# Optimization experiments

Measured on AMD Instinct MI355X. Metric: run time of the kernel, lower is better.

## Reference

```python
import jax, jax.numpy as jnp
import numpy as np
import math

B, C, H, W = 32, 128, 32, 32
NUM_HEADS = 4
GROUPS = 32
EPS = 1e-5


def setup_inputs() -> dict:
    key = jax.random.key(0)
    ks = jax.random.split(key, 6)
    x = jax.random.normal(ks[0], (B, C, H, W), jnp.float32)
    norm_w = 1.0 + 0.1 * jax.random.normal(ks[1], (C,), jnp.float32)
    norm_b = 0.1 * jax.random.normal(ks[2], (C,), jnp.float32)
    qkv_w = jax.random.normal(ks[3], (3 * C, C), jnp.float32) / math.sqrt(C)
    proj_w = jax.random.normal(ks[4], (C, C), jnp.float32) / math.sqrt(C)
    proj_b = 0.01 * jax.random.normal(ks[5], (C,), jnp.float32)
    return {"x": x, "norm_w": norm_w, "norm_b": norm_b, "qkv_w": qkv_w,
            "proj_w": proj_w, "proj_b": proj_b}


def _group_norm(x, w, b):
    b_, c, h, w_ = x.shape
    xg = x.reshape(b_, GROUPS, c // GROUPS, h, w_)
    mu = xg.mean(axis=(2, 3, 4), keepdims=True)
    var = xg.var(axis=(2, 3, 4), keepdims=True)
    xn = ((xg - mu) * jax.lax.rsqrt(var + EPS)).reshape(b_, c, h, w_)
    return xn * w[None, :, None, None] + b[None, :, None, None]


def reference(x, norm_w, norm_b, qkv_w, proj_w, proj_b):
    b, c, h, w = x.shape
    nh = NUM_HEADS
    dh = c // nh
    hw = h * w
    xn = _group_norm(x, norm_w, norm_b)
    # 1x1 conv (no bias): [B,3C,H,W] flattened to [B,3C,HW]
    qkv = jnp.einsum('oc,bchw->bohw', qkv_w, xn).reshape(b, nh, 3 * dh, hw)
    # torch reshape (B*nh, 3C/nh, HW) + chunk(3, dim=1): per-head interleave
    q, k, v = qkv[:, :, :dh], qkv[:, :, dh:2 * dh], qkv[:, :, 2 * dh:]
    scale = 1.0 / math.sqrt(dh)
    # scale applied to BOTH q and k, as in the source
    attn = jnp.einsum('bhct,bhcs->bhts', q * scale, k * scale)  # [B,nh,HW,HW]
    attn = jax.nn.softmax(attn, axis=-1)
    hout = jnp.einsum('bhts,bhcs->bhct', attn, v).reshape(b, c, h, w)
    hout = jnp.einsum('oc,bchw->bohw', proj_w, hout) + proj_b[None, :, None, None]
    return hout + x
```

## Files before the change

kernel.cpp:

```cpp
#include <hip/hip_runtime.h>
#include <math.h>

#define BB 32
#define CC 128
#define HW 1024
#define NG 32
#define TPG 4096
#define QSZ ((size_t)BB * 4 * HW * 32)

typedef __attribute__((ext_vector_type(8))) short fragAB;
typedef __attribute__((ext_vector_type(4))) float fragC;
typedef __attribute__((ext_vector_type(8))) ushort ushort8v;

__device__ __forceinline__ ushort f2bf(float f) {
  union { float f; uint u; } v; v.f = f;
  uint r = v.u + 0x7FFFu + ((v.u >> 16) & 1u);
  return (ushort)(r >> 16);
}
__device__ __forceinline__ uint pack2(float lo, float hi) {
  return __builtin_amdgcn_perm(__float_as_uint(hi), __float_as_uint(lo), 0x07060302u);
}
__device__ __forceinline__ float bflo(uint u) { return __uint_as_float(u << 16); }
__device__ __forceinline__ float bfhi(uint u) { return __uint_as_float(u & 0xffff0000u); }
__device__ __forceinline__ int vswz(int row, int g) {
  return row * 128 + 16 * (g ^ (row & 7));
}

__global__ __launch_bounds__(256) void gn_stats(const float* __restrict__ x,
    float2* __restrict__ stats, const float* __restrict__ qkvw,
    const float* __restrict__ projw, ushort* __restrict__ wq16,
    ushort* __restrict__ wp16) {
  if (blockIdx.x >= 1024) {
    int idx = (blockIdx.x - 1024) * 256 + threadIdx.x;
    if (idx < 49152) wq16[idx] = f2bf(qkvw[idx]);
    else             wp16[idx - 49152] = f2bf(projw[idx - 49152]);
    return;
  }
  int blk = blockIdx.x;
  int b = blk >> 5, g = blk & 31;
  const float4* xp4 = (const float4*)(x + ((size_t)(b * CC + g * 4)) * HW);
  float s = 0.f, s2 = 0.f;
  #pragma unroll
  for (int i = 0; i < 4; ++i) {
    float4 v = xp4[threadIdx.x + i * 256];
    s  += v.x + v.y + v.z + v.w;
    s2 += v.x * v.x + v.y * v.y + v.z * v.z + v.w * v.w;
  }
  #pragma unroll
  for (int off = 32; off; off >>= 1) {
    s  += __shfl_down(s, off, 64);
    s2 += __shfl_down(s2, off, 64);
  }
  __shared__ float ls[4], ls2[4];
  int lane = threadIdx.x & 63, wid = threadIdx.x >> 6;
  if (lane == 0) { ls[wid] = s; ls2[wid] = s2; }
  __syncthreads();
  if (threadIdx.x == 0) {
    float a  = ls[0] + ls[1] + ls[2] + ls[3];
    float a2 = ls2[0] + ls2[1] + ls2[2] + ls2[3];
    float mu = a * (1.f / TPG);
    float var = a2 * (1.f / TPG) - mu * mu;
    stats[blk] = make_float2(mu, rsqrtf(var + 1e-5f));
  }
}

__global__ __launch_bounds__(256) void mgemm_qkv(
    const ushort* __restrict__ W16, const float* __restrict__ xf,
    const float2* __restrict__ stats, const float* __restrict__ gw,
    const float* __restrict__ gb, ushort* __restrict__ Qb) {
  __shared__ ushort Xs[64 * 128];
  int b = blockIdx.z, t0 = blockIdx.x * 64;
  int tid = threadIdx.x;
  int lane = tid & 63, w = tid >> 6, lc = lane & 15, lg = lane >> 4;
  int wo = w >> 1, wt = w & 1;

  {
    int tq = tid & 15, co = tid >> 4;
    const float* xb = xf + (size_t)b * CC * HW + t0 + tq * 4;
    float wsc[8], bsc[8];
    {
      float2 s0 = stats[b * 32 + co * 2];
      float2 s1 = stats[b * 32 + co * 2 + 1];
      #pragma unroll
      for (int cc = 0; cc < 8; ++cc) {
        float rst = (cc < 4) ? s0.y : s1.y;
        float mu  = (cc < 4) ? s0.x : s1.x;
        float g = gw[co * 8 + cc];
        wsc[cc] = g * rst;
        bsc[cc] = gb[co * 8 + cc] - mu * wsc[cc];
      }
    }
    union { float4 v; float f[4]; } vv[8];
    #pragma unroll
    for (int cc = 0; cc < 8; ++cc)
      vv[cc].v = *(const float4*)&xb[(size_t)(co * 8 + cc) * HW];
    #pragma unroll
    for (int tt = 0; tt < 4; ++tt) {
      int row = tq * 4 + tt;
      ushort8v r;
      #pragma unroll
      for (int cc = 0; cc < 8; ++cc)
        r[cc] = f2bf(vv[cc].f[tt] * wsc[cc] + bsc[cc]);
      int byt = (row * 256 + co * 16) ^ ((row & 7) << 4);
      *(ushort8v*)((char*)Xs + byt) = r;
    }
  }
  __syncthreads();

  auto load_af = [&](fragAB af[2][4], int o0) {
    #pragma unroll
    for (int i = 0; i < 2; ++i)
      #pragma unroll
      for (int kc = 0; kc < 4; ++kc)
        af[i][kc] = *(const fragAB*)&W16[(size_t)(o0 + wo * 32 + i * 16 + lc) * 128 + kc * 32 + lg * 8];
  };
  auto kloop = [&](fragAB af[2][4], fragC acc[2][2]) {
    #pragma unroll
    for (int i = 0; i < 2; ++i)
      #pragma unroll
      for (int j = 0; j < 2; ++j)
        acc[i][j] = (fragC){0.f, 0.f, 0.f, 0.f};
    #pragma unroll
    for (int kc = 0; kc < 4; ++kc) {
      fragAB bf[2];
      #pragma unroll
      for (int j = 0; j < 2; ++j) {
        int row = wt * 32 + j * 16 + lc;
        int byt = (row * 256 + kc * 64 + lg * 16) ^ ((row & 7) << 4);
        bf[j] = *(const fragAB*)((const char*)Xs + byt);
      }
      #pragma unroll
      for (int i = 0; i < 2; ++i)
        #pragma unroll
        for (int j = 0; j < 2; ++j)
          acc[i][j] = __builtin_amdgcn_mfma_f32_16x16x32_bf16(af[i][kc], bf[j], acc[i][j], 0, 0, 0);
    }
  };
  auto epi = [&](fragC acc[2][2], int o0) {
    #pragma unroll
    for (int i = 0; i < 2; ++i) {
      int ob = o0 + wo * 32 + i * 16;
      int blk = ob >> 5;
      int hh = blk / 3, kind = blk % 3;
      size_t bh = (size_t)b * 4 + hh;
      float sc = (kind == 0) ? (0.03125f * 1.44269504f) : 1.f;
      #pragma unroll
      for (int j = 0; j < 2; ++j) {
        if (kind < 2) {
          ushort* dst = (kind == 0) ? Qb : (Qb + QSZ);
          int s16 = (t0 >> 4) + wt * 2 + j;
          int eo = s16 * 512 + (((ob & 16) >> 3) + (lg >> 1)) * 128 + lc * 8 + (lg & 1) * 4;
          ushort4 rv;
          rv.x = f2bf(acc[i][j][0] * sc); rv.y = f2bf(acc[i][j][1] * sc);
          rv.z = f2bf(acc[i][j][2] * sc); rv.w = f2bf(acc[i][j][3] * sc);
          *(ushort4*)&dst[bh * 32768 + eo] = rv;
        } else {
          ushort* Vb = Qb + 2 * QSZ;
          int eo = (t0 >> 6) * 2048 + ((ob & 16) >> 4) * 1024
                 + (wt * 4 + j * 2 + (lc >> 3)) * 128 + (lc & 7);
          #pragma unroll
          for (int r = 0; r < 4; ++r)
            Vb[bh * 32768 + eo + (lg * 4 + r) * 8] = f2bf(acc[i][j][r]);
        }
      }
    }
  };

  fragAB afA[2][4], afB[2][4];
  fragC acc[2][2];
  load_af(afA, 0);
  load_af(afB, 64);
  kloop(afA, acc); epi(acc, 0);   load_af(afA, 128);
  kloop(afB, acc); epi(acc, 64);  load_af(afB, 192);
  kloop(afA, acc); epi(acc, 128); load_af(afA, 256);
  kloop(afB, acc); epi(acc, 192); load_af(afB, 320);
  kloop(afA, acc); epi(acc, 256);
  kloop(afB, acc); epi(acc, 320);
}

__global__ __launch_bounds__(512) void attn8(
    const ushort* __restrict__ Qb, const ushort* __restrict__ Kb,
    const ushort* __restrict__ Vb, const ushort* __restrict__ wp16,
    const float* __restrict__ bias, const float* __restrict__ resid,
    float* __restrict__ out) {
  __shared__ char arena[27136];

  int tid = threadIdx.x;
  int w = tid >> 6, lane = tid & 63, lc = lane & 15, lg = lane >> 4;
  int lb = blockIdx.x;
  int gp = (lb & 7) * 128 + (lb >> 3);
  int b = gp >> 5, qt = gp & 31;
  int h = w >> 1, sh = w & 1;
  int bh = b * 4 + h;
  int t0 = qt * 32;

  const ushort* Qg = Qb + (size_t)bh * 32768 + (size_t)qt * 1024 + lane * 8;
  const ushort* Kg = Kb + (size_t)bh * 32768 + lane * 8;
  const ushort* Vg = Vb + (size_t)bh * 32768 + lane * 8;

  fragAB q0 = *(const fragAB*)&Qg[0];
  fragAB q1 = *(const fragAB*)&Qg[512];

  fragC a00 = {0.f,0.f,0.f,0.f}, a01 = {0.f,0.f,0.f,0.f};
  fragC a10 = {0.f,0.f,0.f,0.f}, a11 = {0.f,0.f,0.f,0.f};
  float l0 = 0.f, l1 = 0.f;
  char* PsB = arena + w * 2048;

  for (int i = sh * 8; i < sh * 8 + 8; ++i) {
    const ushort* Kt = Kg + i * 2048;
    const ushort* Vt = Vg + i * 2048;
    fragAB kf[4], vf[4];
    #pragma unroll
    for (int j = 0; j < 4; ++j) kf[j] = *(const fragAB*)&Kt[j * 512];
    #pragma unroll
    for (int u = 0; u < 4; ++u) vf[u] = *(const fragAB*)&Vt[u * 512];

    #pragma unroll
    for (int ts = 0; ts < 2; ++ts) {
      fragAB qf = ts ? q1 : q0;
      fragC S[4];
      #pragma unroll
      for (int j = 0; j < 4; ++j) {
        fragC z = {0.f,0.f,0.f,0.f};
        S[j] = __builtin_amdgcn_mfma_f32_16x16x32_bf16(kf[j], qf, z, 0, 0, 0);
      }
      float rs = 0.f;
      #pragma unroll
      for (int j = 0; j < 4; ++j) {
        float p0 = __builtin_amdgcn_exp2f(S[j][0]), p1 = __builtin_amdgcn_exp2f(S[j][1]);
        float p2 = __builtin_amdgcn_exp2f(S[j][2]), p3 = __builtin_amdgcn_exp2f(S[j][3]);
        rs += (p0 + p1) + (p2 + p3);
        uint2 wv2;
        wv2.x = pack2(p0, p1);
        wv2.y = pack2(p2, p3);
        int g = j * 2 + (lg >> 1);
        *(uint2*)(PsB + lc * 128 + 16 * (g ^ (lc & 7)) + (lg & 1) * 8) = wv2;
      }
      if (ts) l1 += rs; else l0 += rs;
      fragC* aA = ts ? &a01 : &a00;
      fragC* aB = ts ? &a11 : &a10;
      fragAB bp0 = *(const fragAB*)(PsB + vswz(lc, lg));
      fragAB bp1 = *(const fragAB*)(PsB + vswz(lc, 4 + lg));
      *aA = __builtin_amdgcn_mfma_f32_16x16x32_bf16(vf[0], bp0, *aA, 0, 0, 0);
      *aA = __builtin_amdgcn_mfma_f32_16x16x32_bf16(vf[1], bp1, *aA, 0, 0, 0);
      *aB = __builtin_amdgcn_mfma_f32_16x16x32_bf16(vf[2], bp0, *aB, 0, 0, 0);
      *aB = __builtin_amdgcn_mfma_f32_16x16x32_bf16(vf[3], bp1, *aB, 0, 0, 0);
    }
  }

  float2* lpart = (float2*)(arena + 16384);
  if (sh == 1) {
    char* slot = PsB + lane * 32;
    uint2 u;
    u.x = pack2(a00[0], a00[1]); u.y = pack2(a00[2], a00[3]);
    *(uint2*)(slot) = u;
    u.x = pack2(a10[0], a10[1]); u.y = pack2(a10[2], a10[3]);
    *(uint2*)(slot + 8) = u;
    u.x = pack2(a01[0], a01[1]); u.y = pack2(a01[2], a01[3]);
    *(uint2*)(slot + 16) = u;
    u.x = pack2(a11[0], a11[1]); u.y = pack2(a11[2], a11[3]);
    *(uint2*)(slot + 24) = u;
    lpart[h * 64 + lane] = make_float2(l0, l1);
  }
  __syncthreads();

  ushort* Olds = (ushort*)(arena + 18432);
  if (sh == 0) {
    const char* slot = arena + (w + 1) * 2048 + lane * 32;
    uint2 u0 = *(const uint2*)(slot);
    uint2 u1 = *(const uint2*)(slot + 8);
    uint2 u2 = *(const uint2*)(slot + 16);
    uint2 u3 = *(const uint2*)(slot + 24);
    float2 lv = lpart[h * 64 + lane];
    a00[0] += bflo(u0.x); a00[1] += bfhi(u0.x); a00[2] += bflo(u0.y); a00[3] += bfhi(u0.y);
    a10[0] += bflo(u1.x); a10[1] += bfhi(u1.x); a10[2] += bflo(u1.y); a10[3] += bfhi(u1.y);
    a01[0] += bflo(u2.x); a01[1] += bfhi(u2.x); a01[2] += bflo(u2.y); a01[3] += bfhi(u2.y);
    a11[0] += bflo(u3.x); a11[1] += bfhi(u3.x); a11[2] += bflo(u3.y); a11[3] += bfhi(u3.y);
    l0 += lv.x; l1 += lv.y;

    l0 += __shfl_xor(l0, 16); l0 += __shfl_xor(l0, 32);
    l1 += __shfl_xor(l1, 16); l1 += __shfl_xor(l1, 32);
    float il0 = 1.f / l0, il1 = 1.f / l1;

    int cb = h * 32;
    uint2 u;
    u.x = pack2(a00[0] * il0, a00[1] * il0); u.y = pack2(a00[2] * il0, a00[3] * il0);
    *(uint2*)&Olds[lc * 136 + cb + lg * 4] = u;
    u.x = pack2(a10[0] * il0, a10[1] * il0); u.y = pack2(a10[2] * il0, a10[3] * il0);
    *(uint2*)&Olds[lc * 136 + cb + 16 + lg * 4] = u;
    u.x = pack2(a01[0] * il1, a01[1] * il1); u.y = pack2(a01[2] * il1, a01[3] * il1);
    *(uint2*)&Olds[(lc + 16) * 136 + cb + lg * 4] = u;
    u.x = pack2(a11[0] * il1, a11[1] * il1); u.y = pack2(a11[2] * il1, a11[3] * il1);
    *(uint2*)&Olds[(lc + 16) * 136 + cb + 16 + lg * 4] = u;
  }
  __syncthreads();

  fragC pacc[2] = {{0.f,0.f,0.f,0.f}, {0.f,0.f,0.f,0.f}};
  #pragma unroll
  for (int kc = 0; kc < 4; ++kc) {
    fragAB af = *(const fragAB*)&wp16[(size_t)(16 * w + lc) * 128 + kc * 32 + lg * 8];
    #pragma unroll
    for (int j = 0; j < 2; ++j) {
      fragAB bf = *(const fragAB*)&Olds[(j * 16 + lc) * 136 + kc * 32 + lg * 8];
      pacc[j] = __builtin_amdgcn_mfma_f32_16x16x32_bf16(af, bf, pacc[j], 0, 0, 0);
    }
  }
  #pragma unroll
  for (int j = 0; j < 2; ++j) {
    int t = t0 + j * 16 + lc;
    #pragma unroll
    for (int r = 0; r < 4; ++r) {
      int o = 16 * w + lg * 4 + r;
      size_t idx = ((size_t)b * CC + o) * HW + t;
      out[idx] = pacc[j][r] + bias[o] + resid[idx];
    }
  }
}

extern "C" void kernel_launch(void* const* d_in, const int* in_sizes, int n_in,
                              void* d_out, int out_size, void* d_ws, size_t ws_size,
                              hipStream_t stream) {
  (void)in_sizes; (void)n_in; (void)out_size; (void)ws_size;
  const float* x     = (const float*)d_in[0];
  const float* gw    = (const float*)d_in[1];
  const float* gb    = (const float*)d_in[2];
  const float* qkvw  = (const float*)d_in[3];
  const float* projw = (const float*)d_in[4];
  const float* projb = (const float*)d_in[5];
  float* out = (float*)d_out;

  char* wsb = (char*)d_ws;
  ushort* Qb   = (ushort*)(wsb + ((size_t)8 << 20));
  ushort* Kb   = Qb + QSZ;
  ushort* Vb   = Qb + 2 * QSZ;
  ushort* wq16 = (ushort*)(wsb + ((size_t)32 << 20));
  ushort* wp16 = (ushort*)(wsb + ((size_t)32 << 20) + (128 << 10));
  float2* stats = (float2*)(wsb + ((size_t)32 << 20) + (256 << 10));

  gn_stats<<<dim3(BB * NG + 256), 256, 0, stream>>>(x, stats, qkvw, projw, wq16, wp16);
  mgemm_qkv<<<dim3(16, 1, BB), 256, 0, stream>>>(wq16, x, stats, gw, gb, Qb);
  attn8<<<dim3(1024), 512, 0, stream>>>(Qb, Kb, Vb, wp16, projb, x, out);
}
```

Measured before the change: 60.16 us.

## Split attention work by query tile instead of key halves, halving block count

Each attention block now handles 64 queries per batch element, and its two waves per head each take a different 32-query tile over all 16 key tiles. Previously the two waves of a head split the keys and merged partial results through shared memory. Removing that split drops the bf16 partial-accumulator exchange, the extra barrier and the merge arithmetic, and lets the output projection cover 64 tokens per block. The cost is half as many blocks (512 instead of 1024), each doing twice the serial key-loop work, which may reduce latency hiding and occupancy.

```diff
diff --git a/kernel.cpp b/kernel.cpp
--- a/kernel.cpp
+++ b/kernel.cpp
@@ -20,8 +20,6 @@
 __device__ __forceinline__ uint pack2(float lo, float hi) {
   return __builtin_amdgcn_perm(__float_as_uint(hi), __float_as_uint(lo), 0x07060302u);
 }
-__device__ __forceinline__ float bflo(uint u) { return __uint_as_float(u << 16); }
-__device__ __forceinline__ float bfhi(uint u) { return __uint_as_float(u & 0xffff0000u); }
 __device__ __forceinline__ int vswz(int row, int g) {
   return row * 128 + 16 * (g ^ (row & 7));
 }
@@ -178,21 +176,22 @@
   kloop(afB, acc); epi(acc, 320);
 }
 
-__global__ __launch_bounds__(512) void attn8(
+__global__ __launch_bounds__(512) void attn9(
     const ushort* __restrict__ Qb, const ushort* __restrict__ Kb,
     const ushort* __restrict__ Vb, const ushort* __restrict__ wp16,
     const float* __restrict__ bias, const float* __restrict__ resid,
     float* __restrict__ out) {
-  __shared__ char arena[27136];
+  __shared__ char arena[33792];
 
   int tid = threadIdx.x;
   int w = tid >> 6, lane = tid & 63, lc = lane & 15, lg = lane >> 4;
   int lb = blockIdx.x;
-  int gp = (lb & 7) * 128 + (lb >> 3);
-  int b = gp >> 5, qt = gp & 31;
-  int h = w >> 1, sh = w & 1;
+  int gp = (lb & 7) * 64 + (lb >> 3);
+  int b = gp >> 4, qp = gp & 15;
+  int h = w >> 1, qs = w & 1;
   int bh = b * 4 + h;
-  int t0 = qt * 32;
+  int t0 = qp * 64;
+  int qt = qp * 2 + qs;
 
   const ushort* Qg = Qb + (size_t)bh * 32768 + (size_t)qt * 1024 + lane * 8;
   const ushort* Kg = Kb + (size_t)bh * 32768 + lane * 8;
@@ -206,7 +205,7 @@
   float l0 = 0.f, l1 = 0.f;
   char* PsB = arena + w * 2048;
 
-  for (int i = sh * 8; i < sh * 8 + 8; ++i) {
+  for (int i = 0; i < 16; ++i) {
     const ushort* Kt = Kg + i * 2048;
     const ushort* Vt = Vg + i * 2048;
     fragAB kf[4], vf[4];
@@ -248,65 +247,38 @@
     }
   }
 
-  float2* lpart = (float2*)(arena + 16384);
-  if (sh == 1) {
-    char* slot = PsB + lane * 32;
-    uint2 u;
-    u.x = pack2(a00[0], a00[1]); u.y = pack2(a00[2], a00[3]);
-    *(uint2*)(slot) = u;
-    u.x = pack2(a10[0], a10[1]); u.y = pack2(a10[2], a10[3]);
-    *(uint2*)(slot + 8) = u;
-    u.x = pack2(a01[0], a01[1]); u.y = pack2(a01[2], a01[3]);
-    *(uint2*)(slot + 16) = u;
-    u.x = pack2(a11[0], a11[1]); u.y = pack2(a11[2], a11[3]);
-    *(uint2*)(slot + 24) = u;
-    lpart[h * 64 + lane] = make_float2(l0, l1);
-  }
-  __syncthreads();
-
-  ushort* Olds = (ushort*)(arena + 18432);
-  if (sh == 0) {
-    const char* slot = arena + (w + 1) * 2048 + lane * 32;
-    uint2 u0 = *(const uint2*)(slot);
-    uint2 u1 = *(const uint2*)(slot + 8);
-    uint2 u2 = *(const uint2*)(slot + 16);
-    uint2 u3 = *(const uint2*)(slot + 24);
-    float2 lv = lpart[h * 64 + lane];
-    a00[0] += bflo(u0.x); a00[1] += bfhi(u0.x); a00[2] += bflo(u0.y); a00[3] += bfhi(u0.y);
-    a10[0] += bflo(u1.x); a10[1] += bfhi(u1.x); a10[2] += bflo(u1.y); a10[3] += bfhi(u1.y);
-    a01[0] += bflo(u2.x); a01[1] += bfhi(u2.x); a01[2] += bflo(u2.y); a01[3] += bfhi(u2.y);
-    a11[0] += bflo(u3.x); a11[1] += bfhi(u3.x); a11[2] += bflo(u3.y); a11[3] += bfhi(u3.y);
-    l0 += lv.x; l1 += lv.y;
-
-    l0 += __shfl_xor(l0, 16); l0 += __shfl_xor(l0, 32);
-    l1 += __shfl_xor(l1, 16); l1 += __shfl_xor(l1, 32);
-    float il0 = 1.f / l0, il1 = 1.f / l1;
-
-    int cb = h * 32;
+  l0 += __shfl_xor(l0, 16); l0 += __shfl_xor(l0, 32);
+  l1 += __shfl_xor(l1, 16); l1 += __shfl_xor(l1, 32);
+  float il0 = 1.f / l0, il1 = 1.f / l1;
+
+  ushort* Olds = (ushort*)(arena + 16384);
+  {
+    int rb = qs * 32, cb = h * 32;
     uint2 u;
     u.x = pack2(a00[0] * il0, a00[1] * il0); u.y = pack2(a00[2] * il0, a00[3] * il0);
-    *(uint2*)&Olds[lc * 136 + cb + lg * 4] = u;
+    *(uint2*)&Olds[(rb + lc) * 136 + cb + lg * 4] = u;
     u.x = pack2(a10[0] * il0, a10[1] * il0); u.y = pack2(a10[2] * il0, a10[3] * il0);
-    *(uint2*)&Olds[lc * 136 + cb + 16 + lg * 4] = u;
+    *(uint2*)&Olds[(rb + lc) * 136 + cb + 16 + lg * 4] = u;
     u.x = pack2(a01[0] * il1, a01[1] * il1); u.y = pack2(a01[2] * il1, a01[3] * il1);
-    *(uint2*)&Olds[(lc + 16) * 136 + cb + lg * 4] = u;
+    *(uint2*)&Olds[(rb + lc + 16) * 136 + cb + lg * 4] = u;
     u.x = pack2(a11[0] * il1, a11[1] * il1); u.y = pack2(a11[2] * il1, a11[3] * il1);
-    *(uint2*)&Olds[(lc + 16) * 136 + cb + 16 + lg * 4] = u;
+    *(uint2*)&Olds[(rb + lc + 16) * 136 + cb + 16 + lg * 4] = u;
   }
   __syncthreads();
 
-  fragC pacc[2] = {{0.f,0.f,0.f,0.f}, {0.f,0.f,0.f,0.f}};
+  fragC pacc[4] = {{0.f,0.f,0.f,0.f}, {0.f,0.f,0.f,0.f},
+                   {0.f,0.f,0.f,0.f}, {0.f,0.f,0.f,0.f}};
   #pragma unroll
   for (int kc = 0; kc < 4; ++kc) {
     fragAB af = *(const fragAB*)&wp16[(size_t)(16 * w + lc) * 128 + kc * 32 + lg * 8];
     #pragma unroll
-    for (int j = 0; j < 2; ++j) {
+    for (int j = 0; j < 4; ++j) {
       fragAB bf = *(const fragAB*)&Olds[(j * 16 + lc) * 136 + kc * 32 + lg * 8];
       pacc[j] = __builtin_amdgcn_mfma_f32_16x16x32_bf16(af, bf, pacc[j], 0, 0, 0);
     }
   }
   #pragma unroll
-  for (int j = 0; j < 2; ++j) {
+  for (int j = 0; j < 4; ++j) {
     int t = t0 + j * 16 + lc;
     #pragma unroll
     for (int r = 0; r < 4; ++r) {
@@ -339,5 +311,5 @@
 
   gn_stats<<<dim3(BB * NG + 256), 256, 0, stream>>>(x, stats, qkvw, projw, wq16, wp16);
   mgemm_qkv<<<dim3(16, 1, BB), 256, 0, stream>>>(wq16, x, stats, gw, gb, Qb);
-  attn8<<<dim3(1024), 512, 0, stream>>>(Qb, Kb, Vb, wp16, projb, x, out);
-}
+  attn9<<<dim3(512), 512, 0, stream>>>(Qb, Kb, Vb, wp16, projb, x, out);
+}
```

New measurement: 58.49 us (median of 3 runs). 1.03x faster.
